# Kernel tuning notes

Hardware: AMD Instinct MI355X
Metric: run time of the kernel (lower is better)

## Reference

```python
import jax, jax.numpy as jnp
import numpy as np

B = 64        # batch_size (rejection-sampling proposals per column)
P = 200000    # p (number of spike-and-slab variables)
K = 10        # number of accepted samples kept per column
ZETA = 1.1
GAMMA = -0.1
BETA = 2.0 / 3.0
GZ_LOGRATIO = -GAMMA / ZETA


def setup_inputs() -> dict:
    key = jax.random.key(0)
    kZ, kU, ku = jax.random.split(key, 3)
    return {
        "Z": jax.random.normal(kZ, (B, P), dtype=jnp.float32),
        "U": jax.random.uniform(kU, (B, P), dtype=jnp.float32),
        "u": jax.random.uniform(ku, (K, P), dtype=jnp.float32),
        "gamma_alpha": jnp.ones((P,), dtype=jnp.float32),
        "logalpha": jnp.ones((P,), dtype=jnp.float32),
        "batch_size": B,
    }


def reference(Z, U, u, gamma_alpha, logalpha, batch_size):
    # --- MarsagliaTsampler ---
    alpha = jax.nn.relu(gamma_alpha) + 1.0          # [P]
    d = alpha - 1.0 / 3.0                            # [P]
    c = 1.0 / jnp.sqrt(9.0 * d)                      # [P]
    V = (1.0 + c * Z) ** 3                           # [B, P]
    cond1 = Z > -1.0 / c
    cond2 = jnp.log(U) < 0.5 * Z ** 2 + d - d * V + d * jnp.log(V)
    cond = cond1 & cond2                             # nan comparisons -> False, as in torch
    out = jnp.where(cond, d * V, 0.0)                # [B, P]
    # take the FIRST K accepted samples per column (stable compaction)
    order = jnp.where(cond, jnp.arange(batch_size)[:, None], batch_size)
    idx = jnp.argsort(order, axis=0)[:K]             # [K, P]
    theta = jnp.take_along_axis(out, idx, axis=0)    # [K, P]

    # --- hard-concrete spike-and-slab gate (training mode) ---
    z_mean = jax.nn.sigmoid(logalpha - BETA * GZ_LOGRATIO)          # [P]
    s = jax.nn.sigmoid((jnp.log(u) - jnp.log1p(-u) + logalpha) / BETA)  # [K, P]
    z = jnp.clip((ZETA - GAMMA) * s + GAMMA, 0.0, 1.0)              # [K, P]

    return z, z_mean, theta, alpha, logalpha
```

## Files before the change

### kernel.cpp

```cpp
#include <hip/hip_runtime.h>
#include <math.h>

#define KACC 10
#define NRG 4
#define RPG 3
#define SCOLS 64

__global__ __launch_bounds__(256)
void sss_kernel(const float* __restrict__ Z, const float* __restrict__ U,
                const float* __restrict__ uu, const float* __restrict__ ga,
                const float* __restrict__ la, float* __restrict__ out,
                int P, int B, int nbScan, int perK, int vec4)
{
#pragma clang fp contract(off)
    const size_t KP = (size_t)KACC * (size_t)P;
    float* o_z        = out;
    float* o_zmean    = out + KP;
    float* o_theta    = out + KP + (size_t)P;
    float* o_alpha    = out + 2 * KP + (size_t)P;
    float* o_logalpha = out + 2 * KP + 2 * (size_t)P;

    const int bid = blockIdx.x;

    if (bid < nbScan) {
        __shared__ float s_val[NRG * RPG][SCOLS];
        __shared__ int   s_msk[NRG][SCOLS];

        const int t    = threadIdx.x;
        const int lane = t & (SCOLS - 1);
        const int rg   = t >> 6;
        const int col  = bid * SCOLS + lane;
        const bool cok = (col < P);

        const float g = cok ? ga[col] : 1.0f;
        const float alpha = fmaxf(g, 0.0f) + 1.0f;
        const float d     = alpha - (1.0f / 3.0f);
        const float c     = 1.0f / sqrtf(9.0f * d);
        const float neg_inv_c = -(1.0f / c);

        {
            float zv[RPG], wv[RPG];
#pragma unroll
            for (int j = 0; j < RPG; ++j) {
                const int row = rg * RPG + j;
                const size_t off = (size_t)row * (size_t)P + (size_t)col;
                const bool ok = cok && (row < B);
                zv[j] = ok ? Z[off] : __int_as_float(0x7fc00000);
                wv[j] = ok ? U[off] : 1.0f;
            }
            int m = 0;
#pragma unroll
            for (int j = 0; j < RPG; ++j) {
                float z  = zv[j];
                float Uv = wv[j];
                float tt = 1.0f + c * z;
                float V  = (tt * tt) * tt;
                float rhs = ((0.5f * (z * z) + d) - d * V) + d * logf(V);
                bool acc = (z > neg_inv_c) && (logf(Uv) < rhs);
                m |= acc ? (1 << j) : 0;
                s_val[rg * RPG + j][lane] = d * V;
            }
            s_msk[rg][lane] = m;
        }
        __syncthreads();

        const int mask = s_msk[0][lane]
                       | (s_msk[1][lane] << RPG)
                       | (s_msk[2][lane] << (2 * RPG))
                       | (s_msk[3][lane] << (3 * RPG));
        const int pc = __popc(mask);

        if (!__any(pc < KACC)) {
            int m = mask;
            const int skip = rg * RPG;
#pragma unroll
            for (int s = 0; s < (NRG - 1) * RPG; ++s)
                if (s < skip) m &= m - 1;
            const int kcnt = (rg == NRG - 1) ? (KACC - (NRG - 1) * RPG) : RPG;
#pragma unroll
            for (int j = 0; j < RPG; ++j) {
                if (j < kcnt) {
                    const int idx = __ffs(m) - 1;
                    const float v = s_val[idx][lane];
                    if (cok) o_theta[(size_t)(skip + j) * (size_t)P + (size_t)col] = v;
                    m &= m - 1;
                }
            }
            if (rg == NRG - 1 && cok) o_alpha[col] = alpha;
            return;
        }

        if (rg != 0) return;

        float th[KACC];
        {
            int m = mask;
#pragma unroll
            for (int k = 0; k < KACC; ++k) {
                float v = 0.0f;
                if (m) {
                    const int idx = __ffs(m) - 1;
                    v = s_val[idx][lane];
                    m &= m - 1;
                }
                th[k] = v;
            }
        }
        int cnt = (pc > KACC) ? KACC : pc;

        if (cnt < KACC) {
            for (int base = NRG * RPG; base < B; base += 4) {
                float zv[4], wv[4];
#pragma unroll
                for (int i = 0; i < 4; ++i) {
                    const int row = base + i;
                    const size_t off = (size_t)row * (size_t)P + (size_t)col;
                    const bool ok = cok && (row < B);
                    zv[i] = ok ? Z[off] : __int_as_float(0x7fc00000);
                    wv[i] = ok ? U[off] : 1.0f;
                }
#pragma unroll
                for (int i = 0; i < 4; ++i) {
                    float z  = zv[i];
                    float Uv = wv[i];
                    float tt = 1.0f + c * z;
                    float V  = (tt * tt) * tt;
                    float rhs = ((0.5f * (z * z) + d) - d * V) + d * logf(V);
                    bool acc = (z > neg_inv_c) && (logf(Uv) < rhs) && (cnt < KACC);
                    float val = d * V;
#pragma unroll
                    for (int k = 0; k < KACC; ++k)
                        th[k] = (acc && cnt == k) ? val : th[k];
                    cnt += acc ? 1 : 0;
                }
                if (cnt >= KACC) break;
            }
        }

        if (cok) {
#pragma unroll
            for (int k = 0; k < KACC; ++k)
                o_theta[(size_t)k * (size_t)P + (size_t)col] = th[k];
            o_alpha[col] = alpha;
        }

    } else {
        const int gb  = bid - nbScan;
        const int k   = gb / perK;
        const int blk = gb - k * perK;
        const float SHIFT = 0.060606062f;

        if (vec4) {
            const int P4 = P >> 2;
            const int i4 = blk * blockDim.x + threadIdx.x;
            if (i4 >= P4) return;

            const float4 u4  = reinterpret_cast<const float4*>(uu + (size_t)k * (size_t)P)[i4];
            const float4 la4 = reinterpret_cast<const float4*>(la)[i4];

            float4 z4;
            {
                const float* us = (const float*)&u4;
                const float* ls = (const float*)&la4;
                float* zs = (float*)&z4;
#pragma unroll
                for (int j = 0; j < 4; ++j) {
                    float x = ((__logf(us[j]) - __logf(1.0f - us[j])) + ls[j]) * 1.5f;
                    float s = 1.0f / (1.0f + __expf(-x));
                    float zz = 1.2f * s - 0.1f;
                    zs[j] = fminf(fmaxf(zz, 0.0f), 1.0f);
                }
            }
            reinterpret_cast<float4*>(o_z + (size_t)k * (size_t)P)[i4] = z4;

            if (k == 0) {
                const float* ls = (const float*)&la4;
                float4 zm4;
                float* zm = (float*)&zm4;
#pragma unroll
                for (int j = 0; j < 4; ++j)
                    zm[j] = 1.0f / (1.0f + __expf(-(ls[j] - SHIFT)));
                reinterpret_cast<float4*>(o_zmean)[i4]    = zm4;
                reinterpret_cast<float4*>(o_logalpha)[i4] = la4;
            }
        } else {
            const int p = blk * blockDim.x + threadIdx.x;
            if (p >= P) return;
            const float u = uu[(size_t)k * (size_t)P + (size_t)p];
            const float lalpha = la[p];
            float x = ((__logf(u) - __logf(1.0f - u)) + lalpha) * 1.5f;
            float s = 1.0f / (1.0f + __expf(-x));
            float zz = 1.2f * s - 0.1f;
            o_z[(size_t)k * (size_t)P + (size_t)p] = fminf(fmaxf(zz, 0.0f), 1.0f);
            if (k == 0) {
                o_zmean[p]    = 1.0f / (1.0f + __expf(-(lalpha - SHIFT)));
                o_logalpha[p] = lalpha;
            }
        }
    }
}

extern "C" void kernel_launch(void* const* d_in, const int* in_sizes, int n_in,
                              void* d_out, int out_size, void* d_ws, size_t ws_size,
                              hipStream_t stream) {
    const float* Z  = (const float*)d_in[0];
    const float* U  = (const float*)d_in[1];
    const float* uu = (const float*)d_in[2];
    const float* ga = (const float*)d_in[3];
    const float* la = (const float*)d_in[4];
    float* out = (float*)d_out;

    const int P = in_sizes[3];
    const int B = in_sizes[0] / P;
    const int K = in_sizes[2] / P;

    const int block  = 256;
    const int nbScan = (P + SCOLS - 1) / SCOLS;
    const int vec4   = (P % 4 == 0) ? 1 : 0;
    const int perK   = vec4 ? ((P / 4 + block - 1) / block)
                            : ((P + block - 1) / block);
    const int grid   = nbScan + K * perK;
    sss_kernel<<<grid, block, 0, stream>>>(Z, U, uu, ga, la, out, P, B, nbScan, perK, vec4);
}
```

Measured before the change: 16.54 us.

## Widen scan blocks to 256 columns with float4 loads and per-column selection

Each scan block now covers 256 columns instead of 64. In the first phase each thread loads float4 vectors of Z, U and gamma_alpha for 4 adjacent columns across its 3 rows, and packs the acceptance bits into shared memory. In the second phase every thread owns one column, unpacks its 12-bit mask, compacts theta, and falls back to the serial row scan only when fewer than 10 proposals were accepted. This cuts the scan block count by 4x and vectorises the global loads, but it drops the warp-uniform fast path and assumes P is a multiple of 4 with 16-byte-aligned rows in the float4 loads.

```diff
diff --git a/kernel.cpp b/kernel.cpp
--- a/kernel.cpp
+++ b/kernel.cpp
@@ -4,7 +4,8 @@
 #define KACC 10
 #define NRG 4
 #define RPG 3
-#define SCOLS 64
+#define SC  256
+
 
 __global__ __launch_bounds__(256)
 void sss_kernel(const float* __restrict__ Z, const float* __restrict__ U,
@@ -23,74 +24,77 @@
     const int bid = blockIdx.x;
 
     if (bid < nbScan) {
-        __shared__ float s_val[NRG * RPG][SCOLS];
-        __shared__ int   s_msk[NRG][SCOLS];
+        __shared__ float s_val[NRG * RPG][SC];
+        __shared__ int   s_mskp[NRG][SC / 4];
 
         const int t    = threadIdx.x;
-        const int lane = t & (SCOLS - 1);
+        const int lane = t & 63;
         const int rg   = t >> 6;
-        const int col  = bid * SCOLS + lane;
-        const bool cok = (col < P);
-
-        const float g = cok ? ga[col] : 1.0f;
-        const float alpha = fmaxf(g, 0.0f) + 1.0f;
-        const float d     = alpha - (1.0f / 3.0f);
-        const float c     = 1.0f / sqrtf(9.0f * d);
-        const float neg_inv_c = -(1.0f / c);
-
+
+        const int c0  = bid * SC + lane * 4;
+        const bool ok4 = (c0 < P);
+
+        float4 ga4 = ok4 ? *reinterpret_cast<const float4*>(ga + c0)
+                         : make_float4(1.f, 1.f, 1.f, 1.f);
+        float al[4], dd[4], cc[4], nic[4];
         {
-            float zv[RPG], wv[RPG];
-#pragma unroll
-            for (int j = 0; j < RPG; ++j) {
-                const int row = rg * RPG + j;
-                const size_t off = (size_t)row * (size_t)P + (size_t)col;
-                const bool ok = cok && (row < B);
-                zv[j] = ok ? Z[off] : __int_as_float(0x7fc00000);
-                wv[j] = ok ? U[off] : 1.0f;
-            }
-            int m = 0;
-#pragma unroll
-            for (int j = 0; j < RPG; ++j) {
-                float z  = zv[j];
-                float Uv = wv[j];
-                float tt = 1.0f + c * z;
-                float V  = (tt * tt) * tt;
-                float rhs = ((0.5f * (z * z) + d) - d * V) + d * logf(V);
-                bool acc = (z > neg_inv_c) && (logf(Uv) < rhs);
-                m |= acc ? (1 << j) : 0;
-                s_val[rg * RPG + j][lane] = d * V;
-            }
-            s_msk[rg][lane] = m;
-        }
+            const float* gp = (const float*)&ga4;
+#pragma unroll
+            for (int c = 0; c < 4; ++c) {
+                al[c]  = fmaxf(gp[c], 0.0f) + 1.0f;
+                dd[c]  = al[c] - (1.0f / 3.0f);
+                cc[c]  = 1.0f / sqrtf(9.0f * dd[c]);
+                nic[c] = -(1.0f / cc[c]);
+            }
+        }
+
+        int m4[4] = {0, 0, 0, 0};
+#pragma unroll
+        for (int j = 0; j < RPG; ++j) {
+            const int row = rg * RPG + j;
+            const bool ok = ok4 && (row < B);
+            float4 z4, u4;
+            if (ok) {
+                z4 = *reinterpret_cast<const float4*>(Z + (size_t)row * (size_t)P + c0);
+                u4 = *reinterpret_cast<const float4*>(U + (size_t)row * (size_t)P + c0);
+            } else {
+                const float qn = __int_as_float(0x7fc00000);
+                z4 = make_float4(qn, qn, qn, qn);
+                u4 = make_float4(1.f, 1.f, 1.f, 1.f);
+            }
+            float4 v4;
+            {
+                const float* vz = (const float*)&z4;
+                const float* vu = (const float*)&u4;
+                float* vv = (float*)&v4;
+#pragma unroll
+                for (int c = 0; c < 4; ++c) {
+                    float z  = vz[c];
+                    float Uv = vu[c];
+                    float tt = 1.0f + cc[c] * z;
+                    float V  = (tt * tt) * tt;
+                    float rhs = ((0.5f * (z * z) + dd[c]) - dd[c] * V) + dd[c] * logf(V);
+                    bool acc = (z > nic[c]) && (logf(Uv) < rhs);
+                    m4[c] |= acc ? (1 << j) : 0;
+                    vv[c] = dd[c] * V;
+                }
+            }
+            *reinterpret_cast<float4*>(&s_val[rg * RPG + j][lane * 4]) = v4;
+        }
+        s_mskp[rg][lane] = m4[0] | (m4[1] << 3) | (m4[2] << 6) | (m4[3] << 9);
+
+        if (rg == 0 && ok4)
+            *reinterpret_cast<float4*>(o_alpha + c0) = make_float4(al[0], al[1], al[2], al[3]);
+
         __syncthreads();
 
-        const int mask = s_msk[0][lane]
-                       | (s_msk[1][lane] << RPG)
-                       | (s_msk[2][lane] << (2 * RPG))
-                       | (s_msk[3][lane] << (3 * RPG));
-        const int pc = __popc(mask);
-
-        if (!__any(pc < KACC)) {
-            int m = mask;
-            const int skip = rg * RPG;
-#pragma unroll
-            for (int s = 0; s < (NRG - 1) * RPG; ++s)
-                if (s < skip) m &= m - 1;
-            const int kcnt = (rg == NRG - 1) ? (KACC - (NRG - 1) * RPG) : RPG;
-#pragma unroll
-            for (int j = 0; j < RPG; ++j) {
-                if (j < kcnt) {
-                    const int idx = __ffs(m) - 1;
-                    const float v = s_val[idx][lane];
-                    if (cok) o_theta[(size_t)(skip + j) * (size_t)P + (size_t)col] = v;
-                    m &= m - 1;
-                }
-            }
-            if (rg == NRG - 1 && cok) o_alpha[col] = alpha;
-            return;
-        }
-
-        if (rg != 0) return;
+        const int col = bid * SC + t;
+        if (col >= P) return;
+        const int sh = 3 * (t & 3);
+        int mask = 0;
+#pragma unroll
+        for (int r = 0; r < NRG; ++r)
+            mask |= ((s_mskp[r][t >> 2] >> sh) & 7) << (RPG * r);
 
         float th[KACC];
         {
@@ -100,22 +104,28 @@
                 float v = 0.0f;
                 if (m) {
                     const int idx = __ffs(m) - 1;
-                    v = s_val[idx][lane];
+                    v = s_val[idx][t];
                     m &= m - 1;
                 }
                 th[k] = v;
             }
         }
-        int cnt = (pc > KACC) ? KACC : pc;
+        int cnt = __popc(mask);
+        cnt = (cnt > KACC) ? KACC : cnt;
 
         if (cnt < KACC) {
+            const float g = ga[col];
+            const float alpha = fmaxf(g, 0.0f) + 1.0f;
+            const float d  = alpha - (1.0f / 3.0f);
+            const float c  = 1.0f / sqrtf(9.0f * d);
+            const float ni = -(1.0f / c);
             for (int base = NRG * RPG; base < B; base += 4) {
                 float zv[4], wv[4];
 #pragma unroll
                 for (int i = 0; i < 4; ++i) {
                     const int row = base + i;
                     const size_t off = (size_t)row * (size_t)P + (size_t)col;
-                    const bool ok = cok && (row < B);
+                    const bool ok = (row < B);
                     zv[i] = ok ? Z[off] : __int_as_float(0x7fc00000);
                     wv[i] = ok ? U[off] : 1.0f;
                 }
@@ -126,7 +136,7 @@
                     float tt = 1.0f + c * z;
                     float V  = (tt * tt) * tt;
                     float rhs = ((0.5f * (z * z) + d) - d * V) + d * logf(V);
-                    bool acc = (z > neg_inv_c) && (logf(Uv) < rhs) && (cnt < KACC);
+                    bool acc = (z > ni) && (logf(Uv) < rhs) && (cnt < KACC);
                     float val = d * V;
 #pragma unroll
                     for (int k = 0; k < KACC; ++k)
@@ -137,12 +147,9 @@
             }
         }
 
-        if (cok) {
-#pragma unroll
-            for (int k = 0; k < KACC; ++k)
-                o_theta[(size_t)k * (size_t)P + (size_t)col] = th[k];
-            o_alpha[col] = alpha;
-        }
+#pragma unroll
+        for (int k = 0; k < KACC; ++k)
+            o_theta[(size_t)k * (size_t)P + (size_t)col] = th[k];
 
     } else {
         const int gb  = bid - nbScan;
@@ -215,7 +222,7 @@
     const int K = in_sizes[2] / P;
 
     const int block  = 256;
-    const int nbScan = (P + SCOLS - 1) / SCOLS;
+    const int nbScan = (P + SC - 1) / SC;
     const int vec4   = (P % 4 == 0) ? 1 : 0;
     const int perK   = vec4 ? ((P / 4 + block - 1) / block)
                             : ((P + block - 1) / block);
```

Measured after the change: 17.43 us. 1.05x slower.

## Use persistent grid-stride loop interleaving scan and gate tiles 3:2

Applied to the files above, without the earlier changes.

Replaces the one-block-per-tile launch with a fixed 2048-block persistent grid that strides over virtual tiles. Tiles are interleaved so every five contain three rejection-sampling scan tiles and two hard-concrete gate tiles, which mixes memory-heavy and compute work on each CU instead of running all scan blocks before the gate blocks. Gate indexing is flattened across K so each thread handles one float4 of the whole K×P array. This adds loop overhead and an extra block barrier per scan tile, and the 3:2 ratio is tuned to the current sizes.

```diff
diff --git a/kernel.cpp b/kernel.cpp
--- a/kernel.cpp
+++ b/kernel.cpp
@@ -5,12 +5,13 @@
 #define NRG 4
 #define RPG 3
 #define SCOLS 64
+#define GRID 2048
 
 __global__ __launch_bounds__(256)
 void sss_kernel(const float* __restrict__ Z, const float* __restrict__ U,
                 const float* __restrict__ uu, const float* __restrict__ ga,
                 const float* __restrict__ la, float* __restrict__ out,
-                int P, int B, int nbScan, int perK, int vec4)
+                int P, int B, int nS, int nG, int Pq, int vec4, int nT)
 {
 #pragma clang fp contract(off)
     const size_t KP = (size_t)KACC * (size_t)P;
@@ -20,181 +21,190 @@
     float* o_alpha    = out + 2 * KP + (size_t)P;
     float* o_logalpha = out + 2 * KP + 2 * (size_t)P;
 
-    const int bid = blockIdx.x;
-
-    if (bid < nbScan) {
-        __shared__ float s_val[NRG * RPG][SCOLS];
-        __shared__ int   s_msk[NRG][SCOLS];
-
-        const int t    = threadIdx.x;
-        const int lane = t & (SCOLS - 1);
-        const int rg   = t >> 6;
-        const int col  = bid * SCOLS + lane;
-        const bool cok = (col < P);
-
-        const float g = cok ? ga[col] : 1.0f;
-        const float alpha = fmaxf(g, 0.0f) + 1.0f;
-        const float d     = alpha - (1.0f / 3.0f);
-        const float c     = 1.0f / sqrtf(9.0f * d);
-        const float neg_inv_c = -(1.0f / c);
-
-        {
-            float zv[RPG], wv[RPG];
-#pragma unroll
-            for (int j = 0; j < RPG; ++j) {
-                const int row = rg * RPG + j;
-                const size_t off = (size_t)row * (size_t)P + (size_t)col;
-                const bool ok = cok && (row < B);
-                zv[j] = ok ? Z[off] : __int_as_float(0x7fc00000);
-                wv[j] = ok ? U[off] : 1.0f;
-            }
-            int m = 0;
-#pragma unroll
-            for (int j = 0; j < RPG; ++j) {
-                float z  = zv[j];
-                float Uv = wv[j];
-                float tt = 1.0f + c * z;
-                float V  = (tt * tt) * tt;
-                float rhs = ((0.5f * (z * z) + d) - d * V) + d * logf(V);
-                bool acc = (z > neg_inv_c) && (logf(Uv) < rhs);
-                m |= acc ? (1 << j) : 0;
-                s_val[rg * RPG + j][lane] = d * V;
-            }
-            s_msk[rg][lane] = m;
-        }
-        __syncthreads();
-
-        const int mask = s_msk[0][lane]
-                       | (s_msk[1][lane] << RPG)
-                       | (s_msk[2][lane] << (2 * RPG))
-                       | (s_msk[3][lane] << (3 * RPG));
-        const int pc = __popc(mask);
-
-        if (!__any(pc < KACC)) {
-            int m = mask;
-            const int skip = rg * RPG;
-#pragma unroll
-            for (int s = 0; s < (NRG - 1) * RPG; ++s)
-                if (s < skip) m &= m - 1;
-            const int kcnt = (rg == NRG - 1) ? (KACC - (NRG - 1) * RPG) : RPG;
-#pragma unroll
-            for (int j = 0; j < RPG; ++j) {
-                if (j < kcnt) {
-                    const int idx = __ffs(m) - 1;
-                    const float v = s_val[idx][lane];
-                    if (cok) o_theta[(size_t)(skip + j) * (size_t)P + (size_t)col] = v;
-                    m &= m - 1;
-                }
-            }
-            if (rg == NRG - 1 && cok) o_alpha[col] = alpha;
-            return;
-        }
-
-        if (rg != 0) return;
-
-        float th[KACC];
-        {
-            int m = mask;
-#pragma unroll
-            for (int k = 0; k < KACC; ++k) {
-                float v = 0.0f;
-                if (m) {
-                    const int idx = __ffs(m) - 1;
-                    v = s_val[idx][lane];
-                    m &= m - 1;
-                }
-                th[k] = v;
-            }
-        }
-        int cnt = (pc > KACC) ? KACC : pc;
-
-        if (cnt < KACC) {
-            for (int base = NRG * RPG; base < B; base += 4) {
-                float zv[4], wv[4];
-#pragma unroll
-                for (int i = 0; i < 4; ++i) {
-                    const int row = base + i;
+    __shared__ float s_val[NRG * RPG][SCOLS];
+    __shared__ int   s_msk[NRG][SCOLS];
+
+    const int t    = threadIdx.x;
+    const int lane = t & 63;
+    const int rg   = t >> 6;
+    const float SHIFT = 0.060606062f;
+
+    for (int tile = blockIdx.x; tile < nT; tile += GRID) {
+        const int q = tile / 5;
+        const int r = tile - q * 5;
+
+        if (r < 3) {
+            const int s = q * 3 + r;
+            if (s >= nS) continue;
+
+            const int col = s * SCOLS + lane;
+            const bool cok = (col < P);
+
+            const float g = cok ? ga[col] : 1.0f;
+            const float alpha = fmaxf(g, 0.0f) + 1.0f;
+            const float d     = alpha - (1.0f / 3.0f);
+            const float c     = 1.0f / sqrtf(9.0f * d);
+            const float ni    = -(1.0f / c);
+
+            {
+                float zv[RPG], wv[RPG];
+#pragma unroll
+                for (int j = 0; j < RPG; ++j) {
+                    const int row = rg * RPG + j;
                     const size_t off = (size_t)row * (size_t)P + (size_t)col;
                     const bool ok = cok && (row < B);
-                    zv[i] = ok ? Z[off] : __int_as_float(0x7fc00000);
-                    wv[i] = ok ? U[off] : 1.0f;
-                }
-#pragma unroll
-                for (int i = 0; i < 4; ++i) {
-                    float z  = zv[i];
-                    float Uv = wv[i];
+                    zv[j] = ok ? Z[off] : __int_as_float(0x7fc00000);
+                    wv[j] = ok ? U[off] : 1.0f;
+                }
+                int m = 0;
+#pragma unroll
+                for (int j = 0; j < RPG; ++j) {
+                    float z  = zv[j];
+                    float Uv = wv[j];
                     float tt = 1.0f + c * z;
                     float V  = (tt * tt) * tt;
                     float rhs = ((0.5f * (z * z) + d) - d * V) + d * logf(V);
-                    bool acc = (z > neg_inv_c) && (logf(Uv) < rhs) && (cnt < KACC);
-                    float val = d * V;
+                    bool acc = (z > ni) && (logf(Uv) < rhs);
+                    m |= acc ? (1 << j) : 0;
+                    s_val[rg * RPG + j][lane] = d * V;
+                }
+                s_msk[rg][lane] = m;
+            }
+            __syncthreads();
+
+            const int mask = s_msk[0][lane]
+                           | (s_msk[1][lane] << RPG)
+                           | (s_msk[2][lane] << (2 * RPG))
+                           | (s_msk[3][lane] << (3 * RPG));
+            const int pc = __popc(mask);
+
+            if (!__any(pc < KACC)) {
+                int m = mask;
+                const int skip = rg * RPG;
+#pragma unroll
+                for (int s2 = 0; s2 < (NRG - 1) * RPG; ++s2)
+                    if (s2 < skip) m &= m - 1;
+                const int kcnt = (rg == NRG - 1) ? (KACC - (NRG - 1) * RPG) : RPG;
+#pragma unroll
+                for (int j = 0; j < RPG; ++j) {
+                    if (j < kcnt) {
+                        const int idx = __ffs(m) - 1;
+                        const float v = s_val[idx][lane];
+                        if (cok) o_theta[(size_t)(skip + j) * (size_t)P + (size_t)col] = v;
+                        m &= m - 1;
+                    }
+                }
+                if (rg == NRG - 1 && cok) o_alpha[col] = alpha;
+            } else if (rg == 0) {
+                float th[KACC];
+                {
+                    int m = mask;
+#pragma unroll
+                    for (int k = 0; k < KACC; ++k) {
+                        float v = 0.0f;
+                        if (m) {
+                            const int idx = __ffs(m) - 1;
+                            v = s_val[idx][lane];
+                            m &= m - 1;
+                        }
+                        th[k] = v;
+                    }
+                }
+                int cnt = (pc > KACC) ? KACC : pc;
+
+                if (cnt < KACC) {
+                    for (int base = NRG * RPG; base < B; base += 4) {
+                        float zv[4], wv[4];
+#pragma unroll
+                        for (int i = 0; i < 4; ++i) {
+                            const int row = base + i;
+                            const size_t off = (size_t)row * (size_t)P + (size_t)col;
+                            const bool ok = cok && (row < B);
+                            zv[i] = ok ? Z[off] : __int_as_float(0x7fc00000);
+                            wv[i] = ok ? U[off] : 1.0f;
+                        }
+#pragma unroll
+                        for (int i = 0; i < 4; ++i) {
+                            float z  = zv[i];
+                            float Uv = wv[i];
+                            float tt = 1.0f + c * z;
+                            float V  = (tt * tt) * tt;
+                            float rhs = ((0.5f * (z * z) + d) - d * V) + d * logf(V);
+                            bool acc = (z > ni) && (logf(Uv) < rhs) && (cnt < KACC);
+                            float val = d * V;
+#pragma unroll
+                            for (int k = 0; k < KACC; ++k)
+                                th[k] = (acc && cnt == k) ? val : th[k];
+                            cnt += acc ? 1 : 0;
+                        }
+                        if (cnt >= KACC) break;
+                    }
+                }
+
+                if (cok) {
 #pragma unroll
                     for (int k = 0; k < KACC; ++k)
-                        th[k] = (acc && cnt == k) ? val : th[k];
-                    cnt += acc ? 1 : 0;
-                }
-                if (cnt >= KACC) break;
+                        o_theta[(size_t)k * (size_t)P + (size_t)col] = th[k];
+                    o_alpha[col] = alpha;
+                }
             }
-        }
-
-        if (cok) {
-#pragma unroll
-            for (int k = 0; k < KACC; ++k)
-                o_theta[(size_t)k * (size_t)P + (size_t)col] = th[k];
-            o_alpha[col] = alpha;
-        }
-
-    } else {
-        const int gb  = bid - nbScan;
-        const int k   = gb / perK;
-        const int blk = gb - k * perK;
-        const float SHIFT = 0.060606062f;
-
-        if (vec4) {
-            const int P4 = P >> 2;
-            const int i4 = blk * blockDim.x + threadIdx.x;
-            if (i4 >= P4) return;
-
-            const float4 u4  = reinterpret_cast<const float4*>(uu + (size_t)k * (size_t)P)[i4];
-            const float4 la4 = reinterpret_cast<const float4*>(la)[i4];
-
-            float4 z4;
-            {
-                const float* us = (const float*)&u4;
-                const float* ls = (const float*)&la4;
-                float* zs = (float*)&z4;
-#pragma unroll
-                for (int j = 0; j < 4; ++j) {
-                    float x = ((__logf(us[j]) - __logf(1.0f - us[j])) + ls[j]) * 1.5f;
-                    float s = 1.0f / (1.0f + __expf(-x));
-                    float zz = 1.2f * s - 0.1f;
-                    zs[j] = fminf(fmaxf(zz, 0.0f), 1.0f);
-                }
-            }
-            reinterpret_cast<float4*>(o_z + (size_t)k * (size_t)P)[i4] = z4;
-
-            if (k == 0) {
-                const float* ls = (const float*)&la4;
-                float4 zm4;
-                float* zm = (float*)&zm4;
-#pragma unroll
-                for (int j = 0; j < 4; ++j)
-                    zm[j] = 1.0f / (1.0f + __expf(-(ls[j] - SHIFT)));
-                reinterpret_cast<float4*>(o_zmean)[i4]    = zm4;
-                reinterpret_cast<float4*>(o_logalpha)[i4] = la4;
-            }
+            __syncthreads();
+
         } else {
-            const int p = blk * blockDim.x + threadIdx.x;
-            if (p >= P) return;
-            const float u = uu[(size_t)k * (size_t)P + (size_t)p];
-            const float lalpha = la[p];
-            float x = ((__logf(u) - __logf(1.0f - u)) + lalpha) * 1.5f;
-            float s = 1.0f / (1.0f + __expf(-x));
-            float zz = 1.2f * s - 0.1f;
-            o_z[(size_t)k * (size_t)P + (size_t)p] = fminf(fmaxf(zz, 0.0f), 1.0f);
-            if (k == 0) {
-                o_zmean[p]    = 1.0f / (1.0f + __expf(-(lalpha - SHIFT)));
-                o_logalpha[p] = lalpha;
+            const int gidx = q * 2 + (r - 3);
+            if (gidx >= nG) continue;
+
+            if (vec4) {
+                const int idx = gidx * 256 + t;
+                if (idx < KACC * Pq) {
+                    const int k  = idx / Pq;
+                    const int i4 = idx - k * Pq;
+
+                    const float4 u4  = reinterpret_cast<const float4*>(uu)[idx];
+                    const float4 la4 = reinterpret_cast<const float4*>(la)[i4];
+
+                    float4 z4;
+                    {
+                        const float* us = (const float*)&u4;
+                        const float* ls = (const float*)&la4;
+                        float* zs = (float*)&z4;
+#pragma unroll
+                        for (int j = 0; j < 4; ++j) {
+                            float x = ((__logf(us[j]) - __logf(1.0f - us[j])) + ls[j]) * 1.5f;
+                            float sg = 1.0f / (1.0f + __expf(-x));
+                            float zz = 1.2f * sg - 0.1f;
+                            zs[j] = fminf(fmaxf(zz, 0.0f), 1.0f);
+                        }
+                    }
+                    reinterpret_cast<float4*>(o_z)[idx] = z4;
+
+                    if (k == 0) {
+                        const float* ls = (const float*)&la4;
+                        float4 zm4;
+                        float* zm = (float*)&zm4;
+#pragma unroll
+                        for (int j = 0; j < 4; ++j)
+                            zm[j] = 1.0f / (1.0f + __expf(-(ls[j] - SHIFT)));
+                        reinterpret_cast<float4*>(o_zmean)[i4]    = zm4;
+                        reinterpret_cast<float4*>(o_logalpha)[i4] = la4;
+                    }
+                }
+            } else {
+                const int idx = gidx * 256 + t;
+                if (idx < KACC * P) {
+                    const int k = idx / P;
+                    const int p = idx - k * P;
+                    const float u = uu[idx];
+                    const float lalpha = la[p];
+                    float x = ((__logf(u) - __logf(1.0f - u)) + lalpha) * 1.5f;
+                    float sg = 1.0f / (1.0f + __expf(-x));
+                    float zz = 1.2f * sg - 0.1f;
+                    o_z[idx] = fminf(fmaxf(zz, 0.0f), 1.0f);
+                    if (k == 0) {
+                        o_zmean[p]    = 1.0f / (1.0f + __expf(-(lalpha - SHIFT)));
+                        o_logalpha[p] = lalpha;
+                    }
+                }
             }
         }
     }
@@ -212,13 +222,16 @@
 
     const int P = in_sizes[3];
     const int B = in_sizes[0] / P;
-    const int K = in_sizes[2] / P;
-
-    const int block  = 256;
-    const int nbScan = (P + SCOLS - 1) / SCOLS;
-    const int vec4   = (P % 4 == 0) ? 1 : 0;
-    const int perK   = vec4 ? ((P / 4 + block - 1) / block)
-                            : ((P + block - 1) / block);
-    const int grid   = nbScan + K * perK;
-    sss_kernel<<<grid, block, 0, stream>>>(Z, U, uu, ga, la, out, P, B, nbScan, perK, vec4);
+
+    const int vec4 = (P % 4 == 0) ? 1 : 0;
+    const int Pq   = P / 4;
+    const int nS   = (P + SCOLS - 1) / SCOLS;
+    const int nG   = vec4 ? (KACC * Pq + 255) / 256
+                          : (KACC * P  + 255) / 256;
+    const int tS = ((nS + 2) / 3) * 5;
+    const int tG = ((nG + 1) / 2) * 5;
+    const int nT = (tS > tG) ? tS : tG;
+
+    sss_kernel<<<GRID, 256, 0, stream>>>(Z, U, uu, ga, la, out, P, B,
+                                         nS, nG, Pq, vec4, nT);
 }
```

Result: slower. 22.41 us (+35.5%).

## Fuse gate computation into scan blocks, dropping separate gate block range

Applied to the files above, without the earlier changes.

Removes the separate set of blocks that computed the hard-concrete gate z, z_mean and logalpha. Each 64-column scan block now also computes the gate for its own 10x64 tile, issuing the u/logalpha loads alongside the Z/U loads before the sync. This cuts the grid size and overlaps the gate work with the rejection-sampling scan. The cost is that gate loads are scalar rather than float4, and each scan block does more work and uses more registers.

```diff
diff --git a/kernel.cpp b/kernel.cpp
--- a/kernel.cpp
+++ b/kernel.cpp
@@ -5,12 +5,14 @@
 #define NRG 4
 #define RPG 3
 #define SCOLS 64
+#define GE (SCOLS * KACC)
+
 
 __global__ __launch_bounds__(256)
 void sss_kernel(const float* __restrict__ Z, const float* __restrict__ U,
                 const float* __restrict__ uu, const float* __restrict__ ga,
                 const float* __restrict__ la, float* __restrict__ out,
-                int P, int B, int nbScan, int perK, int vec4)
+                int P, int B)
 {
 #pragma clang fp contract(off)
     const size_t KP = (size_t)KACC * (size_t)P;
@@ -20,183 +22,159 @@
     float* o_alpha    = out + 2 * KP + (size_t)P;
     float* o_logalpha = out + 2 * KP + 2 * (size_t)P;
 
-    const int bid = blockIdx.x;
+    __shared__ float s_val[NRG * RPG][SCOLS];
+    __shared__ int   s_msk[NRG][SCOLS];
 
-    if (bid < nbScan) {
-        __shared__ float s_val[NRG * RPG][SCOLS];
-        __shared__ int   s_msk[NRG][SCOLS];
+    const int bid  = blockIdx.x;
+    const int t    = threadIdx.x;
+    const int lane = t & 63;
+    const int rg   = t >> 6;
+    const int col0 = bid * SCOLS;
+    const int col  = col0 + lane;
+    const bool cok = (col < P);
+    const float SHIFT = 0.060606062f;
 
-        const int t    = threadIdx.x;
-        const int lane = t & (SCOLS - 1);
-        const int rg   = t >> 6;
-        const int col  = bid * SCOLS + lane;
-        const bool cok = (col < P);
+    const float g = cok ? ga[col] : 1.0f;
+    float zv[RPG], wv[RPG];
+#pragma unroll
+    for (int j = 0; j < RPG; ++j) {
+        const int row = rg * RPG + j;
+        const size_t off = (size_t)row * (size_t)P + (size_t)col;
+        const bool ok = cok && (row < B);
+        zv[j] = ok ? Z[off] : __int_as_float(0x7fc00000);
+        wv[j] = ok ? U[off] : 1.0f;
+    }
+    float guv[3], glv[3];
+    int   gk[3], gc[3];
+    bool  gok[3];
+#pragma unroll
+    for (int i = 0; i < 3; ++i) {
+        const int e = t + i * 256;
+        gk[i]  = e >> 6;
+        gc[i]  = e & 63;
+        gok[i] = (e < GE) && (col0 + gc[i] < P);
+        const size_t uoff = (size_t)gk[i] * (size_t)P + (size_t)(col0 + gc[i]);
+        guv[i] = gok[i] ? uu[uoff] : 0.5f;
+        glv[i] = gok[i] ? la[col0 + gc[i]] : 0.0f;
+    }
 
-        const float g = cok ? ga[col] : 1.0f;
-        const float alpha = fmaxf(g, 0.0f) + 1.0f;
-        const float d     = alpha - (1.0f / 3.0f);
-        const float c     = 1.0f / sqrtf(9.0f * d);
-        const float neg_inv_c = -(1.0f / c);
+    const float alpha = fmaxf(g, 0.0f) + 1.0f;
+    const float d     = alpha - (1.0f / 3.0f);
+    const float c     = 1.0f / sqrtf(9.0f * d);
+    const float ni    = -(1.0f / c);
+    {
+        int m = 0;
+#pragma unroll
+        for (int j = 0; j < RPG; ++j) {
+            float z  = zv[j];
+            float Uv = wv[j];
+            float tt = 1.0f + c * z;
+            float V  = (tt * tt) * tt;
+            float rhs = ((0.5f * (z * z) + d) - d * V) + d * logf(V);
+            bool acc = (z > ni) && (logf(Uv) < rhs);
+            m |= acc ? (1 << j) : 0;
+            s_val[rg * RPG + j][lane] = d * V;
+        }
+        s_msk[rg][lane] = m;
+    }
 
-        {
-            float zv[RPG], wv[RPG];
 #pragma unroll
-            for (int j = 0; j < RPG; ++j) {
-                const int row = rg * RPG + j;
+    for (int i = 0; i < 3; ++i) {
+        if (gok[i]) {
+            float u = guv[i];
+            float x = ((__logf(u) - __logf(1.0f - u)) + glv[i]) * 1.5f;
+            float s = 1.0f / (1.0f + __expf(-x));
+            float zz = 1.2f * s - 0.1f;
+            o_z[(size_t)gk[i] * (size_t)P + (size_t)(col0 + gc[i])] =
+                fminf(fmaxf(zz, 0.0f), 1.0f);
+        }
+    }
+    if (t < SCOLS && cok) {
+        const float l = la[col];
+        o_zmean[col]    = 1.0f / (1.0f + __expf(-(l - SHIFT)));
+        o_logalpha[col] = l;
+    }
+
+    __syncthreads();
+
+    const int mask = s_msk[0][lane]
+                   | (s_msk[1][lane] << RPG)
+                   | (s_msk[2][lane] << (2 * RPG))
+                   | (s_msk[3][lane] << (3 * RPG));
+    const int pc = __popc(mask);
+
+    if (!__any(pc < KACC)) {
+        int m = mask;
+        const int skip = rg * RPG;
+#pragma unroll
+        for (int s = 0; s < (NRG - 1) * RPG; ++s)
+            if (s < skip) m &= m - 1;
+        const int kcnt = (rg == NRG - 1) ? (KACC - (NRG - 1) * RPG) : RPG;
+#pragma unroll
+        for (int j = 0; j < RPG; ++j) {
+            if (j < kcnt) {
+                const int idx = __ffs(m) - 1;
+                const float v = s_val[idx][lane];
+                if (cok) o_theta[(size_t)(skip + j) * (size_t)P + (size_t)col] = v;
+                m &= m - 1;
+            }
+        }
+        if (rg == NRG - 1 && cok) o_alpha[col] = alpha;
+        return;
+    }
+
+    if (rg != 0) return;
+
+    float th[KACC];
+    {
+        int m = mask;
+#pragma unroll
+        for (int k = 0; k < KACC; ++k) {
+            float v = 0.0f;
+            if (m) {
+                const int idx = __ffs(m) - 1;
+                v = s_val[idx][lane];
+                m &= m - 1;
+            }
+            th[k] = v;
+        }
+    }
+    int cnt = (pc > KACC) ? KACC : pc;
+
+    if (cnt < KACC) {
+        for (int base = NRG * RPG; base < B; base += 4) {
+            float zv2[4], wv2[4];
+#pragma unroll
+            for (int i = 0; i < 4; ++i) {
+                const int row = base + i;
                 const size_t off = (size_t)row * (size_t)P + (size_t)col;
                 const bool ok = cok && (row < B);
-                zv[j] = ok ? Z[off] : __int_as_float(0x7fc00000);
-                wv[j] = ok ? U[off] : 1.0f;
+                zv2[i] = ok ? Z[off] : __int_as_float(0x7fc00000);
+                wv2[i] = ok ? U[off] : 1.0f;
             }
-            int m = 0;
 #pragma unroll
-            for (int j = 0; j < RPG; ++j) {
-                float z  = zv[j];
-                float Uv = wv[j];
+            for (int i = 0; i < 4; ++i) {
+                float z  = zv2[i];
+                float Uv = wv2[i];
                 float tt = 1.0f + c * z;
                 float V  = (tt * tt) * tt;
                 float rhs = ((0.5f * (z * z) + d) - d * V) + d * logf(V);
-                bool acc = (z > neg_inv_c) && (logf(Uv) < rhs);
-                m |= acc ? (1 << j) : 0;
-                s_val[rg * RPG + j][lane] = d * V;
+                bool acc = (z > ni) && (logf(Uv) < rhs) && (cnt < KACC);
+                float val = d * V;
+#pragma unroll
+                for (int k = 0; k < KACC; ++k)
+                    th[k] = (acc && cnt == k) ? val : th[k];
+                cnt += acc ? 1 : 0;
             }
-            s_msk[rg][lane] = m;
+            if (cnt >= KACC) break;
         }
-        __syncthreads();
+    }
 
-        const int mask = s_msk[0][lane]
-                       | (s_msk[1][lane] << RPG)
-                       | (s_msk[2][lane] << (2 * RPG))
-                       | (s_msk[3][lane] << (3 * RPG));
-        const int pc = __popc(mask);
-
-        if (!__any(pc < KACC)) {
-            int m = mask;
-            const int skip = rg * RPG;
+    if (cok) {
 #pragma unroll
-            for (int s = 0; s < (NRG - 1) * RPG; ++s)
-                if (s < skip) m &= m - 1;
-            const int kcnt = (rg == NRG - 1) ? (KACC - (NRG - 1) * RPG) : RPG;
-#pragma unroll
-            for (int j = 0; j < RPG; ++j) {
-                if (j < kcnt) {
-                    const int idx = __ffs(m) - 1;
-                    const float v = s_val[idx][lane];
-                    if (cok) o_theta[(size_t)(skip + j) * (size_t)P + (size_t)col] = v;
-                    m &= m - 1;
-                }
-            }
-            if (rg == NRG - 1 && cok) o_alpha[col] = alpha;
-            return;
-        }
-
-        if (rg != 0) return;
-
-        float th[KACC];
-        {
-            int m = mask;
-#pragma unroll
-            for (int k = 0; k < KACC; ++k) {
-                float v = 0.0f;
-                if (m) {
-                    const int idx = __ffs(m) - 1;
-                    v = s_val[idx][lane];
-                    m &= m - 1;
-                }
-                th[k] = v;
-            }
-        }
-        int cnt = (pc > KACC) ? KACC : pc;
-
-        if (cnt < KACC) {
-            for (int base = NRG * RPG; base < B; base += 4) {
-                float zv[4], wv[4];
-#pragma unroll
-                for (int i = 0; i < 4; ++i) {
-                    const int row = base + i;
-                    const size_t off = (size_t)row * (size_t)P + (size_t)col;
-                    const bool ok = cok && (row < B);
-                    zv[i] = ok ? Z[off] : __int_as_float(0x7fc00000);
-                    wv[i] = ok ? U[off] : 1.0f;
-                }
-#pragma unroll
-                for (int i = 0; i < 4; ++i) {
-                    float z  = zv[i];
-                    float Uv = wv[i];
-                    float tt = 1.0f + c * z;
-                    float V  = (tt * tt) * tt;
-                    float rhs = ((0.5f * (z * z) + d) - d * V) + d * logf(V);
-                    bool acc = (z > neg_inv_c) && (logf(Uv) < rhs) && (cnt < KACC);
-                    float val = d * V;
-#pragma unroll
-                    for (int k = 0; k < KACC; ++k)
-                        th[k] = (acc && cnt == k) ? val : th[k];
-                    cnt += acc ? 1 : 0;
-                }
-                if (cnt >= KACC) break;
-            }
-        }
-
-        if (cok) {
-#pragma unroll
-            for (int k = 0; k < KACC; ++k)
-                o_theta[(size_t)k * (size_t)P + (size_t)col] = th[k];
-            o_alpha[col] = alpha;
-        }
-
-    } else {
-        const int gb  = bid - nbScan;
-        const int k   = gb / perK;
-        const int blk = gb - k * perK;
-        const float SHIFT = 0.060606062f;
-
-        if (vec4) {
-            const int P4 = P >> 2;
-            const int i4 = blk * blockDim.x + threadIdx.x;
-            if (i4 >= P4) return;
-
-            const float4 u4  = reinterpret_cast<const float4*>(uu + (size_t)k * (size_t)P)[i4];
-            const float4 la4 = reinterpret_cast<const float4*>(la)[i4];
-
-            float4 z4;
-            {
-                const float* us = (const float*)&u4;
-                const float* ls = (const float*)&la4;
-                float* zs = (float*)&z4;
-#pragma unroll
-                for (int j = 0; j < 4; ++j) {
-                    float x = ((__logf(us[j]) - __logf(1.0f - us[j])) + ls[j]) * 1.5f;
-                    float s = 1.0f / (1.0f + __expf(-x));
-                    float zz = 1.2f * s - 0.1f;
-                    zs[j] = fminf(fmaxf(zz, 0.0f), 1.0f);
-                }
-            }
-            reinterpret_cast<float4*>(o_z + (size_t)k * (size_t)P)[i4] = z4;
-
-            if (k == 0) {
-                const float* ls = (const float*)&la4;
-                float4 zm4;
-                float* zm = (float*)&zm4;
-#pragma unroll
-                for (int j = 0; j < 4; ++j)
-                    zm[j] = 1.0f / (1.0f + __expf(-(ls[j] - SHIFT)));
-                reinterpret_cast<float4*>(o_zmean)[i4]    = zm4;
-                reinterpret_cast<float4*>(o_logalpha)[i4] = la4;
-            }
-        } else {
-            const int p = blk * blockDim.x + threadIdx.x;
-            if (p >= P) return;
-            const float u = uu[(size_t)k * (size_t)P + (size_t)p];
-            const float lalpha = la[p];
-            float x = ((__logf(u) - __logf(1.0f - u)) + lalpha) * 1.5f;
-            float s = 1.0f / (1.0f + __expf(-x));
-            float zz = 1.2f * s - 0.1f;
-            o_z[(size_t)k * (size_t)P + (size_t)p] = fminf(fmaxf(zz, 0.0f), 1.0f);
-            if (k == 0) {
-                o_zmean[p]    = 1.0f / (1.0f + __expf(-(lalpha - SHIFT)));
-                o_logalpha[p] = lalpha;
-            }
-        }
+        for (int k = 0; k < KACC; ++k)
+            o_theta[(size_t)k * (size_t)P + (size_t)col] = th[k];
+        o_alpha[col] = alpha;
     }
 }
 
@@ -212,13 +190,7 @@
 
     const int P = in_sizes[3];
     const int B = in_sizes[0] / P;
-    const int K = in_sizes[2] / P;
 
-    const int block  = 256;
-    const int nbScan = (P + SCOLS - 1) / SCOLS;
-    const int vec4   = (P % 4 == 0) ? 1 : 0;
-    const int perK   = vec4 ? ((P / 4 + block - 1) / block)
-                            : ((P + block - 1) / block);
-    const int grid   = nbScan + K * perK;
-    sss_kernel<<<grid, block, 0, stream>>>(Z, U, uu, ga, la, out, P, B, nbScan, perK, vec4);
+    const int grid = (P + SCOLS - 1) / SCOLS;
+    sss_kernel<<<grid, 256, 0, stream>>>(Z, U, uu, ga, la, out, P, B);
 }
```

After: 18.83 us. 13.9% more time.
